# Performance work log

Hardware: AMD Instinct MI355X
Metric: run time of the kernel (lower is better)

## Reference

```python
import jax, jax.numpy as jnp
import numpy as np

H = 8  # num_heads


def _ln(x, g, b):
    mu = x.mean(-1, keepdims=True)
    var = ((x - mu) ** 2).mean(-1, keepdims=True)
    return (x - mu) * jax.lax.rsqrt(var + 1e-5) * g + b


def setup_inputs() -> dict:
    key = jax.random.key(0)
    ks = jax.random.split(key, 24)
    B, N, V, E, D, R, L = 8, 512, 50000, 300, 256, 100, 4
    dh = D // H
    s = 0.02
    inp = {}
    inp['token_ids'] = jax.random.randint(ks[0], (B, N), 0, V, dtype=jnp.int32)
    inp['relations'] = jax.random.randint(ks[1], (B, N, N), 0, R, dtype=jnp.int32)
    m = jax.random.bernoulli(ks[2], 0.9, (B, N, N))
    eye = jnp.eye(N, dtype=bool)[None]
    inp['relations_mask'] = jnp.logical_or(m, eye)  # keep diagonal valid so every row attends somewhere
    inp['embed'] = jax.random.normal(ks[3], (V, E), jnp.float32) * s
    inp['W_in'] = jax.random.normal(ks[4], (E, D), jnp.float32) * s
    inp['b_in'] = jnp.zeros((D,), jnp.float32)
    inp['Wq'] = jax.random.normal(ks[5], (L, D, D), jnp.float32) * s
    inp['Wk'] = jax.random.normal(ks[6], (L, D, D), jnp.float32) * s
    inp['Wv'] = jax.random.normal(ks[7], (L, D, D), jnp.float32) * s
    inp['Wo'] = jax.random.normal(ks[8], (L, D, D), jnp.float32) * s
    inp['ln1_g'] = jnp.ones((L, D), jnp.float32)
    inp['ln1_b'] = jnp.zeros((L, D), jnp.float32)
    inp['ln2_g'] = jnp.ones((L, D), jnp.float32)
    inp['ln2_b'] = jnp.zeros((L, D), jnp.float32)
    inp['W1'] = jax.random.normal(ks[9], (L, D, 4 * D), jnp.float32) * s
    inp['b1'] = jnp.zeros((L, 4 * D), jnp.float32)
    inp['W2'] = jax.random.normal(ks[10], (L, 4 * D, D), jnp.float32) * s
    inp['b2'] = jnp.zeros((L, D), jnp.float32)
    inp['rel_k_emb'] = jax.random.normal(ks[11], (R, dh), jnp.float32) * s
    inp['rel_v_emb'] = jax.random.normal(ks[12], (R, dh), jnp.float32) * s
    inp['W_out'] = jax.random.normal(ks[13], (D, D), jnp.float32) * s
    inp['b_out'] = jnp.zeros((D,), jnp.float32)
    return inp


def reference(token_ids, relations, relations_mask, embed, W_in, b_in, Wq, Wk, Wv, Wo,
              ln1_g, ln1_b, ln2_g, ln2_b, W1, b1, W2, b2, rel_k_emb, rel_v_emb, W_out, b_out):
    # Input layer: embedding lookup + projection to gnn hidden size.
    x = embed[token_ids]                          # [B,N,E]
    x = jax.nn.relu(x @ W_in + b_in)              # [B,N,D]
    B, N, D = x.shape
    dh = D // H
    # Shared relation embeddings (share_layers=True, share_heads=True): gathered once.
    rk = rel_k_emb[relations]                     # [B,N,N,dh]
    rv = rel_v_emb[relations]                     # [B,N,N,dh]
    neg = jnp.asarray(-1e9, x.dtype)
    scale = jnp.asarray(1.0 / np.sqrt(dh), x.dtype)
    L = Wq.shape[0]
    for l in range(L):  # fixed small layer count
        q = (x @ Wq[l]).reshape(B, N, H, dh).transpose(0, 2, 1, 3)
        k = (x @ Wk[l]).reshape(B, N, H, dh).transpose(0, 2, 1, 3)
        v = (x @ Wv[l]).reshape(B, N, H, dh).transpose(0, 2, 1, 3)
        # Relation-aware scores: q.k + q.r_k (RAT-SQL)
        scores = (jnp.einsum('bhnd,bhmd->bhnm', q, k)
                  + jnp.einsum('bhnd,bnmd->bhnm', q, rk)) * scale
        scores = jnp.where(relations_mask[:, None], scores, neg)
        a = jax.nn.softmax(scores, axis=-1)       # [B,H,N,N]
        z = (jnp.einsum('bhnm,bhmd->bhnd', a, v)
             + jnp.einsum('bhnm,bnmd->bhnd', a, rv))
        z = z.transpose(0, 2, 1, 3).reshape(B, N, D) @ Wo[l]
        x = _ln(x + z, ln1_g[l], ln1_b[l])
        f = jax.nn.relu(x @ W1[l] + b1[l]) @ W2[l] + b2[l]
        x = _ln(x + f, ln2_g[l], ln2_b[l])
    # Output layer projection
    return x @ W_out + b_out
```

## Files before the change

kernel.cpp:

```cpp
#include <hip/hip_runtime.h>
#include <hip/hip_bf16.h>

#define NTOK 4096
#define NN   512

typedef __attribute__((ext_vector_type(8))) short bf16x8;
typedef __attribute__((ext_vector_type(4))) float f32x4;
typedef __attribute__((ext_vector_type(4))) unsigned short u16x4;

__device__ __forceinline__ float bf16_to_f(unsigned short u) {
    unsigned int x = ((unsigned int)u) << 16;
    return __builtin_bit_cast(float, x);
}
__device__ __forceinline__ unsigned short f_to_bf16(float f) {
    unsigned int b = __builtin_bit_cast(unsigned int, f);
    return (unsigned short)((b + 0x7fff + ((b >> 16) & 1)) >> 16);
}
__device__ __forceinline__ bf16x8 pack8(float4 a, float4 b) {
    bf16x8 v;
    v[0]=(short)f_to_bf16(a.x); v[1]=(short)f_to_bf16(a.y);
    v[2]=(short)f_to_bf16(a.z); v[3]=(short)f_to_bf16(a.w);
    v[4]=(short)f_to_bf16(b.x); v[5]=(short)f_to_bf16(b.y);
    v[6]=(short)f_to_bf16(b.z); v[7]=(short)f_to_bf16(b.w);
    return v;
}

__global__ void detect_mask_kernel(const unsigned char* __restrict__ m, int* __restrict__ flag) {
    __shared__ int f;
    if (threadIdx.x == 0) f = 0;
    __syncthreads();
    int any = 0;
    for (int i = threadIdx.x; i < 4096; i += 256) {
        if ((i & 3) != 0 && m[i] != 0) any = 1;
    }
    if (any) atomicOr(&f, 1);
    __syncthreads();
    if (threadIdx.x == 0) *flag = f;
}

__global__ __launch_bounds__(256) void prep_rel16(
    const int* __restrict__ rel, const void* __restrict__ mask,
    const int* __restrict__ flag, short* __restrict__ rel16)
{
    const bool mbyte = (*flag != 0);
    const unsigned char* m8 = (const unsigned char*)mask;
    const int* m32 = (const int*)mask;
    const int i = (blockIdx.x * 256 + threadIdx.x) * 2;
    int2 rv = *(const int2*)(rel + i);
    int ok0, ok1;
    if (mbyte) { ok0 = m8[i]; ok1 = m8[i + 1]; }
    else       { ok0 = (m32[i] != 0); ok1 = (m32[i + 1] != 0); }
    short2 o;
    o.x = ok0 ? (short)rv.x : (short)-1;
    o.y = ok1 ? (short)rv.y : (short)-1;
    *(short2*)(rel16 + i) = o;
}

__global__ __launch_bounds__(256) void tcast256(
    const float* __restrict__ Wq, const float* __restrict__ Wk,
    const float* __restrict__ Wv, const float* __restrict__ Wo,
    const float* __restrict__ Wout, unsigned short* __restrict__ wt,
    int nL, float scale)
{
    const int z = blockIdx.z;
    const float* src; unsigned short* dst; float sc = 1.f;
    if (z >= nL * 4) {
        src = Wout; dst = wt + (size_t)nL * 786432;
    } else {
        const int l = z >> 2, which = z & 3;
        if      (which == 0) { src = Wq + (size_t)l * 65536; sc = scale; }
        else if (which == 1) { src = Wk + (size_t)l * 65536; }
        else if (which == 2) { src = Wv + (size_t)l * 65536; }
        else                 { src = Wo + (size_t)l * 65536; }
        dst = wt + (size_t)l * 786432 + which * 65536;
    }
    __shared__ float tile[32][33];
    const int t = threadIdx.x, tx = t & 31, ty = t >> 5;
    const int n0 = blockIdx.x * 32, k0 = blockIdx.y * 32;
#pragma unroll
    for (int p = 0; p < 4; ++p)
        tile[ty + p * 8][tx] = src[(size_t)(k0 + ty + p * 8) * 256 + n0 + tx];
    __syncthreads();
#pragma unroll
    for (int p = 0; p < 4; ++p)
        dst[(size_t)(n0 + ty + p * 8) * 256 + k0 + tx] = f_to_bf16(tile[tx][ty + p * 8] * sc);
}

__global__ __launch_bounds__(256) void tcastKN(
    const float* __restrict__ in, unsigned short* __restrict__ out,
    int K, int N, long inStride, long outStride)
{
    in  += (size_t)blockIdx.z * inStride;
    out += (size_t)blockIdx.z * outStride;
    __shared__ float tile[32][33];
    const int t = threadIdx.x, tx = t & 31, ty = t >> 5;
    const int n0 = blockIdx.x * 32, k0 = blockIdx.y * 32;
#pragma unroll
    for (int p = 0; p < 4; ++p)
        tile[ty + p * 8][tx] = in[(size_t)(k0 + ty + p * 8) * N + n0 + tx];
    __syncthreads();
#pragma unroll
    for (int p = 0; p < 4; ++p)
        out[(size_t)(n0 + ty + p * 8) * K + k0 + tx] = f_to_bf16(tile[tx][ty + p * 8]);
}

__global__ __launch_bounds__(256) void embed_proj_kernel(
    const int* __restrict__ tok, const float* __restrict__ embed,
    const float* __restrict__ W_in, const float* __restrict__ b_in,
    float* __restrict__ x, unsigned short* __restrict__ xh)
{
    __shared__ float emb[8][304];
    __shared__ int tloc[8];
    const int t = threadIdx.x;
    const int r0 = blockIdx.x * 8;
    if (t < 8) tloc[t] = tok[r0 + t];
    __syncthreads();
    for (int i = t; i < 8 * 300; i += 256) {
        int r = i / 300, e = i - r * 300;
        emb[r][e] = embed[(size_t)tloc[r] * 300 + e];
    }
    __syncthreads();
    float acc[8] = {0.f,0.f,0.f,0.f,0.f,0.f,0.f,0.f};
    const int d = t;
    for (int e = 0; e < 300; ++e) {
        float w = W_in[e * 256 + d];
#pragma unroll
        for (int r = 0; r < 8; ++r) acc[r] += emb[r][e] * w;
    }
    const float bb = b_in[d];
#pragma unroll
    for (int r = 0; r < 8; ++r) {
        float o = acc[r] + bb;
        o = o > 0.f ? o : 0.f;
        x[(size_t)(r0 + r) * 256 + d] = o;
        xh[(size_t)(r0 + r) * 256 + d] = f_to_bf16(o);
    }
}

__global__ __launch_bounds__(256) void gemm_bf16_64(
    const unsigned short* __restrict__ A, const unsigned short* __restrict__ WT,
    const float* __restrict__ bias, float* __restrict__ Cf, unsigned short* __restrict__ Ch,
    int M, int K, int Nc, int relu)
{
    __shared__ unsigned short As[2][64][40];
    __shared__ unsigned short Bs[2][64][40];
    const int t = threadIdx.x;
    const int lane = t & 63, w = t >> 6;
    const int g = lane >> 4, li = lane & 15;
    const int r0 = blockIdx.y * 64, c0 = blockIdx.x * 64;

    f32x4 acc[4];
#pragma unroll
    for (int i = 0; i < 4; ++i) acc[i] = (f32x4){0.f,0.f,0.f,0.f};

    const int arow = t >> 2, ad8 = (t & 3) * 8;

    bf16x8 a0 = *(const bf16x8*)(A  + (size_t)(r0 + arow) * K + ad8);
    bf16x8 b0 = *(const bf16x8*)(WT + (size_t)(c0 + arow) * K + ad8);

    const int nk = K >> 5;
    for (int ki = 0; ki < nk; ++ki) {
        const int cur = ki & 1;
        *(bf16x8*)&As[cur][arow][ad8] = a0;
        *(bf16x8*)&Bs[cur][arow][ad8] = b0;
        if (ki + 1 < nk) {
            const int k0 = (ki + 1) * 32;
            a0 = *(const bf16x8*)(A  + (size_t)(r0 + arow) * K + k0 + ad8);
            b0 = *(const bf16x8*)(WT + (size_t)(c0 + arow) * K + k0 + ad8);
        }
        __syncthreads();
        bf16x8 af = *(const bf16x8*)&As[cur][16 * w + li][g * 8];
#pragma unroll
        for (int sub = 0; sub < 4; ++sub) {
            bf16x8 bfr = *(const bf16x8*)&Bs[cur][16 * sub + li][g * 8];
            acc[sub] = __builtin_amdgcn_mfma_f32_16x16x32_bf16(af, bfr, acc[sub], 0, 0, 0);
        }
    }
#pragma unroll
    for (int sub = 0; sub < 4; ++sub) {
        int col = c0 + sub * 16 + li;
        float bv = bias ? bias[col] : 0.f;
#pragma unroll
        for (int r = 0; r < 4; ++r) {
            int row = r0 + 16 * w + g * 4 + r;
            float o = acc[sub][r] + bv;
            if (relu) o = fmaxf(o, 0.f);
            if (Ch) Ch[(size_t)row * Nc + col] = f_to_bf16(o);
            else    Cf[(size_t)row * Nc + col] = o;
        }
    }
}

__global__ __launch_bounds__(256) void gemm_bf16_32(
    const unsigned short* __restrict__ A, const unsigned short* __restrict__ WT,
    const float* __restrict__ bias, float* __restrict__ Cf, unsigned short* __restrict__ Ch,
    int M, int K, int Nc, int relu)
{
    __shared__ unsigned short As[2][32][40];
    __shared__ unsigned short Bs[2][64][40];
    const int t = threadIdx.x;
    const int lane = t & 63, w = t >> 6;
    const int g = lane >> 4, li = lane & 15;
    const int r0 = blockIdx.y * 32, c0 = blockIdx.x * 64;

    f32x4 acc[2];
    acc[0] = (f32x4){0.f,0.f,0.f,0.f};
    acc[1] = (f32x4){0.f,0.f,0.f,0.f};

    const int arow = t >> 3, a4 = (t & 7) * 4;
    const int bcol = t >> 2, bk8 = (t & 3) * 8;

    u16x4 a0 = *(const u16x4*)(A + (size_t)(r0 + arow) * K + a4);
    bf16x8 b0 = *(const bf16x8*)(WT + (size_t)(c0 + bcol) * K + bk8);

    const int nk = K >> 5;
    for (int ki = 0; ki < nk; ++ki) {
        const int cur = ki & 1;
        *(u16x4*)&As[cur][arow][a4] = a0;
        *(bf16x8*)&Bs[cur][bcol][bk8] = b0;
        if (ki + 1 < nk) {
            const int k0 = (ki + 1) * 32;
            a0 = *(const u16x4*)(A + (size_t)(r0 + arow) * K + k0 + a4);
            b0 = *(const bf16x8*)(WT + (size_t)(c0 + bcol) * K + k0 + bk8);
        }
        __syncthreads();
        bf16x8 af = *(const bf16x8*)&As[cur][16 * (w & 1) + li][g * 8];
#pragma unroll
        for (int sub = 0; sub < 2; ++sub) {
            bf16x8 bfr = *(const bf16x8*)&Bs[cur][(w >> 1) * 32 + sub * 16 + li][g * 8];
            acc[sub] = __builtin_amdgcn_mfma_f32_16x16x32_bf16(af, bfr, acc[sub], 0, 0, 0);
        }
    }
#pragma unroll
    for (int sub = 0; sub < 2; ++sub) {
        int col = c0 + (w >> 1) * 32 + sub * 16 + li;
        float bv = bias ? bias[col] : 0.f;
#pragma unroll
        for (int r = 0; r < 4; ++r) {
            int row = r0 + 16 * (w & 1) + g * 4 + r;
            float o = acc[sub][r] + bv;
            if (relu) o = fmaxf(o, 0.f);
            if (Ch) Ch[(size_t)row * Nc + col] = f_to_bf16(o);
            else    Cf[(size_t)row * Nc + col] = o;
        }
    }
}

__global__ __launch_bounds__(256) void qrk_kernel(
    const unsigned short* __restrict__ qkvh, const float* __restrict__ relk_g,
    unsigned short* __restrict__ qrkg)
{
    const int n0 = blockIdx.x * 64, h = blockIdx.y, b = blockIdx.z;
    const int t = threadIdx.x, lane = t & 63, w = t >> 6;
    const int g = lane >> 4, li = lane & 15;
    const int qrow = 16 * w + g * 4;

    __shared__ unsigned short relk_s[100][40];
    for (int i = t; i < 400; i += 256) {
        int rr = i >> 2, d8 = (i & 3) * 8;
        const float* sp = relk_g + rr * 32 + d8;
        *(bf16x8*)&relk_s[rr][d8] = pack8(*(const float4*)sp, *(const float4*)(sp + 4));
    }
    bf16x8 qf = *(const bf16x8*)(qkvh + (size_t)(b * NN + n0 + 16 * w + li) * 768 + h * 32 + g * 8);
    __syncthreads();
#pragma unroll
    for (int rc = 0; rc < 7; ++rc) {
        bf16x8 bb = *(const bf16x8*)&relk_s[rc * 16 + li][g * 8];
        f32x4 s = __builtin_amdgcn_mfma_f32_16x16x32_bf16(qf, bb, (f32x4){0.f,0.f,0.f,0.f}, 0, 0, 0);
        int col = rc * 16 + li;
        if (col < 100) {
#pragma unroll
            for (int r = 0; r < 4; ++r)
                qrkg[((size_t)(b * 8 + h) * NN + n0 + qrow + r) * 100 + col] = f_to_bf16(s[r]);
        }
    }
}

__global__ __launch_bounds__(256, 4) void attn_mfma(
    const unsigned short* __restrict__ qkvh,
    const short* __restrict__ rel16,
    const unsigned short* __restrict__ qrkg,
    const float* __restrict__ relv_g,
    float* __restrict__ zpart, float* __restrict__ smpart)
{
    const int p = blockIdx.x;
    const int cx = p & 7, k = p >> 3;
    const int sg = cx * 16 + (k >> 3);
    const int h  = k & 7;
    const int b = sg >> 4, chunk = sg & 15;
    const int n0 = chunk * 32;

    const int t = threadIdx.x;
    const int lane = t & 63, w = t >> 6;
    const int qw = w & 1, mhalf = w >> 1;
    const int g = lane >> 4, li = lane & 15;
    const int qrow = 16 * qw + g * 4;
    const int mbase = mhalf * 256;

    __shared__ float wrel[32][100];
    __shared__ unsigned short qrk_lds[32][100];
    __shared__ union {
        unsigned short relvT[32][136];
        struct {
            unsigned short v_t[2][2][32][40];
            unsigned short p_s[4][16][40];
        } mn;
    } u;

    for (int i = t; i < 3200; i += 256) ((float*)wrel)[i] = 0.f;
    {
        const unsigned short* qsrc = qrkg + ((size_t)(b * 8 + h) * NN + n0) * 100;
        for (int i = t; i < 1600; i += 256) {
            int row = i / 50, off = (i - row * 50) * 2;
            *(unsigned int*)&qrk_lds[row][off] =
                *(const unsigned int*)(qsrc + (size_t)row * 100 + off);
        }
    }
    bf16x8 qf = *(const bf16x8*)(qkvh + (size_t)(b * NN + n0 + 16 * qw + li) * 768 + h * 32 + g * 8);

    const short* relrow[4];
#pragma unroll
    for (int r = 0; r < 4; ++r)
        relrow[r] = rel16 + ((size_t)b * NN + n0 + qrow + r) * NN;
    const int th = t & 127;
    const int vm = th & 31, vdg = th >> 5;
    const size_t kRB = (size_t)(b * NN) * 768 + 256 + h * 32 + g * 8;
    const size_t vRB = (size_t)(b * NN) * 768 + 512 + h * 32 + vdg * 8;

    bf16x8 kbuf[2][2]; bf16x8 vbuf[2]; short rbuf[2][8];
#pragma unroll
    for (int i = 0; i < 8; ++i)
        rbuf[0][i] = relrow[i & 3][mbase + (i >> 2) * 16 + li];
    kbuf[0][0] = *(const bf16x8*)(qkvh + kRB + (size_t)(mbase + li) * 768);
    kbuf[0][1] = *(const bf16x8*)(qkvh + kRB + (size_t)(mbase + 16 + li) * 768);
    vbuf[0]    = *(const bf16x8*)(qkvh + vRB + (size_t)(mbase + vm) * 768);

    float smacc[4] = {0.f, 0.f, 0.f, 0.f};
    f32x4 zf[2];
    zf[0] = (f32x4){0.f,0.f,0.f,0.f};
    zf[1] = (f32x4){0.f,0.f,0.f,0.f};

#pragma unroll
    for (int tt = 0; tt < 8; ++tt) {
        const int cur = tt & 1, nxt = cur ^ 1;
        {
            bf16x8 vv = vbuf[cur];
#pragma unroll
            for (int j = 0; j < 8; ++j)
                u.mn.v_t[mhalf][cur][vdg * 8 + j][vm] = (unsigned short)vv[j];
        }
        if (tt + 1 < 8) {
            const int m0n = mbase + (tt + 1) * 32;
#pragma unroll
            for (int i = 0; i < 8; ++i)
                rbuf[nxt][i] = relrow[i & 3][m0n + (i >> 2) * 16 + li];
        }
        __syncthreads();
        bf16x8 kf0 = kbuf[cur][0], kf1 = kbuf[cur][1];
        if (tt + 1 < 8) {
            const int m0n = mbase + (tt + 1) * 32;
            kbuf[nxt][0] = *(const bf16x8*)(qkvh + kRB + (size_t)(m0n + li) * 768);
            kbuf[nxt][1] = *(const bf16x8*)(qkvh + kRB + (size_t)(m0n + 16 + li) * 768);
            vbuf[nxt]    = *(const bf16x8*)(qkvh + vRB + (size_t)(m0n + vm) * 768);
        }
        f32x4 s0 = __builtin_amdgcn_mfma_f32_16x16x32_bf16(qf, kf0, (f32x4){0.f,0.f,0.f,0.f}, 0, 0, 0);
        f32x4 s1 = __builtin_amdgcn_mfma_f32_16x16x32_bf16(qf, kf1, (f32x4){0.f,0.f,0.f,0.f}, 0, 0, 0);
        float pr[8];
#pragma unroll
        for (int i = 0; i < 8; ++i) {
            const int r = i & 3;
            const int rl = rbuf[cur][i];
            const float qadd = bf16_to_f(qrk_lds[qrow + r][rl < 0 ? 0 : rl]);
            const float sv = ((i >> 2) ? s1[r] : s0[r]) + qadd;
            float pv = 0.f;
            if (rl >= 0) {
                pv = __expf(fminf(sv, 50.f));
                atomicAdd(&wrel[qrow + r][rl], pv);
            }
            smacc[r] += pv;
            pr[i] = pv;
        }
#pragma unroll
        for (int i = 0; i < 8; ++i)
            u.mn.p_s[w][g * 4 + (i & 3)][(i >> 2) * 16 + li] = f_to_bf16(pr[i]);
        asm volatile("s_waitcnt lgkmcnt(0)" ::: "memory");
        __builtin_amdgcn_sched_barrier(0);
        bf16x8 pa = *(const bf16x8*)&u.mn.p_s[w][li][g * 8];
#pragma unroll
        for (int dc = 0; dc < 2; ++dc) {
            bf16x8 vb = *(const bf16x8*)&u.mn.v_t[mhalf][cur][dc * 16 + li][g * 8];
            zf[dc] = __builtin_amdgcn_mfma_f32_16x16x32_bf16(pa, vb, zf[dc], 0, 0, 0);
        }
    }
    __syncthreads();

    for (int i = t; i < 32 * 36; i += 256) {
        int d = i / 36, c = 100 + (i - (i / 36) * 36);
        u.relvT[d][c] = 0;
    }
    for (int i = t; i < 400; i += 256) {
        int rr2 = i >> 2, d8 = (i & 3) * 8;
        const float* sp = relv_g + rr2 * 32 + d8;
        float4 s0 = *(const float4*)sp, s1 = *(const float4*)(sp + 4);
        u.relvT[d8 + 0][rr2] = f_to_bf16(s0.x);
        u.relvT[d8 + 1][rr2] = f_to_bf16(s0.y);
        u.relvT[d8 + 2][rr2] = f_to_bf16(s0.z);
        u.relvT[d8 + 3][rr2] = f_to_bf16(s0.w);
        u.relvT[d8 + 4][rr2] = f_to_bf16(s1.x);
        u.relvT[d8 + 5][rr2] = f_to_bf16(s1.y);
        u.relvT[d8 + 6][rr2] = f_to_bf16(s1.z);
        u.relvT[d8 + 7][rr2] = f_to_bf16(s1.w);
    }
    __syncthreads();
    if (mhalf == 0) {
#pragma unroll
        for (int kc = 0; kc < 4; ++kc) {
            const int kbase = kc * 32 + g * 8;
            const float* wp = &wrel[16 * qw + li][0];
            bf16x8 af;
#pragma unroll
            for (int j = 0; j < 8; ++j) {
                int id = kbase + j;
                float val = (id < 100) ? wp[id] : 0.f;
                af[j] = (short)f_to_bf16(val);
            }
#pragma unroll
            for (int dc = 0; dc < 2; ++dc) {
                bf16x8 vbr = *(const bf16x8*)&u.relvT[dc * 16 + li][kbase];
                zf[dc] = __builtin_amdgcn_mfma_f32_16x16x32_bf16(af, vbr, zf[dc], 0, 0, 0);
            }
        }
    }
#pragma unroll
    for (int r = 0; r < 4; ++r) {
        smacc[r] += __shfl_xor(smacc[r], 1, 64);
        smacc[r] += __shfl_xor(smacc[r], 2, 64);
        smacc[r] += __shfl_xor(smacc[r], 4, 64);
        smacc[r] += __shfl_xor(smacc[r], 8, 64);
    }
#pragma unroll
    for (int r = 0; r < 4; ++r) {
        const int row = b * NN + n0 + qrow + r;
        size_t ob = (size_t)mhalf * 1048576 + (size_t)row * 256 + h * 32;
#pragma unroll
        for (int dc = 0; dc < 2; ++dc)
            zpart[ob + dc * 16 + li] = zf[dc][r];
        if (li == 0)
            smpart[(size_t)mhalf * 32768 + (size_t)row * 8 + h] = smacc[r];
    }
}

__global__ __launch_bounds__(256) void combine_kernel(
    const float* __restrict__ zpart, const float* __restrict__ smpart,
    unsigned short* __restrict__ zbf)
{
    const int t = threadIdx.x;
    const int wi = t >> 6, lane = t & 63;
    const int row = blockIdx.x * 4 + wi;
    const int h = lane >> 3;
    float den = 0.f;
    float4 acc = make_float4(0.f, 0.f, 0.f, 0.f);
#pragma unroll
    for (int s = 0; s < 2; ++s) {
        den += smpart[(size_t)s * 32768 + (size_t)row * 8 + h];
        float4 v = *(const float4*)(zpart + (size_t)s * 1048576 + (size_t)row * 256 + lane * 4);
        acc.x += v.x; acc.y += v.y; acc.z += v.z; acc.w += v.w;
    }
    const float inv = 1.f / den;
    u16x4 oh;
    oh[0] = f_to_bf16(acc.x * inv);
    oh[1] = f_to_bf16(acc.y * inv);
    oh[2] = f_to_bf16(acc.z * inv);
    oh[3] = f_to_bf16(acc.w * inv);
    *(u16x4*)(zbf + (size_t)row * 256 + lane * 4) = oh;
}

__global__ __launch_bounds__(256) void ln_kernel(
    const float* __restrict__ xin, const float* __restrict__ y,
    const float* __restrict__ g, const float* __restrict__ bsh,
    float* __restrict__ xout, unsigned short* __restrict__ xh)
{
    const int t = threadIdx.x;
    const int w = t >> 6, lane = t & 63;
    const size_t row = (size_t)blockIdx.x * 4 + w;
    const float4 xv = *(const float4*)(xin + row * 256 + lane * 4);
    const float4 yv = *(const float4*)(y + row * 256 + lane * 4);
    float4 sv;
    sv.x = xv.x + yv.x; sv.y = xv.y + yv.y; sv.z = xv.z + yv.z; sv.w = xv.w + yv.w;
    float sum = sv.x + sv.y + sv.z + sv.w;
    float sq  = sv.x * sv.x + sv.y * sv.y + sv.z * sv.z + sv.w * sv.w;
#pragma unroll
    for (int off = 1; off < 64; off <<= 1) {
        sum += __shfl_xor(sum, off, 64);
        sq  += __shfl_xor(sq, off, 64);
    }
    const float mu = sum * (1.f / 256.f);
    const float var = sq * (1.f / 256.f) - mu * mu;
    const float rs = rsqrtf(var + 1e-5f);
    const float4 gv = *(const float4*)(g + lane * 4);
    const float4 bv = *(const float4*)(bsh + lane * 4);
    float4 o;
    o.x = (sv.x - mu) * rs * gv.x + bv.x;
    o.y = (sv.y - mu) * rs * gv.y + bv.y;
    o.z = (sv.z - mu) * rs * gv.z + bv.z;
    o.w = (sv.w - mu) * rs * gv.w + bv.w;
    *(float4*)(xout + row * 256 + lane * 4) = o;
    u16x4 oh;
    oh[0] = f_to_bf16(o.x); oh[1] = f_to_bf16(o.y);
    oh[2] = f_to_bf16(o.z); oh[3] = f_to_bf16(o.w);
    *(u16x4*)(xh + row * 256 + lane * 4) = oh;
}

extern "C" void kernel_launch(void* const* d_in, const int* in_sizes, int n_in,
                              void* d_out, int out_size, void* d_ws, size_t ws_size,
                              hipStream_t stream)
{
    (void)in_sizes; (void)n_in; (void)out_size;
    const int*   tok   = (const int*)d_in[0];
    const int*   rel   = (const int*)d_in[1];
    const void*  mask  = d_in[2];
    const float* embed = (const float*)d_in[3];
    const float* W_in  = (const float*)d_in[4];
    const float* b_in  = (const float*)d_in[5];
    const float* Wq    = (const float*)d_in[6];
    const float* Wk    = (const float*)d_in[7];
    const float* Wv    = (const float*)d_in[8];
    const float* Wo    = (const float*)d_in[9];
    const float* ln1g  = (const float*)d_in[10];
    const float* ln1b  = (const float*)d_in[11];
    const float* ln2g  = (const float*)d_in[12];
    const float* ln2b  = (const float*)d_in[13];
    const float* W1    = (const float*)d_in[14];
    const float* b1    = (const float*)d_in[15];
    const float* W2    = (const float*)d_in[16];
    const float* b2    = (const float*)d_in[17];
    const float* relk  = (const float*)d_in[18];
    const float* relv  = (const float*)d_in[19];
    const float* Wout  = (const float*)d_in[20];
    const float* bout  = (const float*)d_in[21];
    float* out = (float*)d_out;
    const float scale = 0.17677669529663687f;

    float* ws = (float*)d_ws;
    float*          x     = ws;
    unsigned short* xh    = (unsigned short*)(ws + 1048576);
    unsigned short* zbf   = (unsigned short*)(ws + 1572864);
    float*          zo    = ws + 2097152;
    unsigned short* qkvh  = (unsigned short*)(ws + 3145728);
    unsigned short* hbh   = (unsigned short*)(ws + 4718592);
    float*          zpart = ws + 6815744;
    float*          smpart= ws + 8912896;
    unsigned short* qrkg  = (unsigned short*)(ws + 8978432);
    int*            flag  = (int*)(ws + 10616832);
    unsigned short* wt    = (unsigned short*)(ws + 10616848);

    const size_t wsf = ws_size >> 2;
    const bool tierA = wsf >= 13271100;
    short* rel16 = tierA ? (short*)(ws + 12222480) : (short*)hbh;

    detect_mask_kernel<<<1, 256, 0, stream>>>((const unsigned char*)mask, flag);
    embed_proj_kernel<<<512, 256, 0, stream>>>(tok, embed, W_in, b_in, x, xh);
    if (tierA) {
        prep_rel16<<<4096, 256, 0, stream>>>(rel, mask, flag, rel16);
        tcast256<<<dim3(8, 8, 17), 256, 0, stream>>>(Wq, Wk, Wv, Wo, Wout, wt, 4, scale);
        tcastKN<<<dim3(32, 8, 4), 256, 0, stream>>>(W1, wt + 262144, 256, 1024, 262144, 786432);
        tcastKN<<<dim3(8, 32, 4), 256, 0, stream>>>(W2, wt + 524288, 1024, 256, 262144, 786432);
    }

    for (int l = 0; l < 4; ++l) {
        unsigned short* wl = tierA ? wt + (size_t)l * 786432 : wt;
        if (!tierA) {
            prep_rel16<<<4096, 256, 0, stream>>>(rel, mask, flag, rel16);
            tcast256<<<dim3(8, 8, 4), 256, 0, stream>>>(
                Wq + (size_t)l * 65536, Wk + (size_t)l * 65536,
                Wv + (size_t)l * 65536, Wo + (size_t)l * 65536, Wout, wt, 1, scale);
            tcastKN<<<dim3(32, 8, 1), 256, 0, stream>>>(W1 + (size_t)l * 262144, wt + 262144, 256, 1024, 0, 0);
            tcastKN<<<dim3(8, 32, 1), 256, 0, stream>>>(W2 + (size_t)l * 262144, wt + 524288, 1024, 256, 0, 0);
        }
        gemm_bf16_64<<<dim3(12, 64), 256, 0, stream>>>(xh, wl, nullptr, nullptr, qkvh,
                                                       NTOK, 256, 768, 0);
        qrk_kernel<<<dim3(8, 8, 8), 256, 0, stream>>>(qkvh, relk, qrkg);
        attn_mfma<<<1024, 256, 0, stream>>>(qkvh, rel16, qrkg, relv, zpart, smpart);
        combine_kernel<<<1024, 256, 0, stream>>>(zpart, smpart, zbf);
        gemm_bf16_32<<<dim3(4, 128), 256, 0, stream>>>(zbf, wl + 196608, nullptr, zo, nullptr,
                                                       NTOK, 256, 256, 0);
        ln_kernel<<<1024, 256, 0, stream>>>(x, zo, ln1g + l * 256, ln1b + l * 256, x, xh);
        gemm_bf16_64<<<dim3(16, 64), 256, 0, stream>>>(xh, wl + 262144, b1 + l * 1024, nullptr, hbh,
                                                       NTOK, 256, 1024, 1);
        gemm_bf16_32<<<dim3(4, 128), 256, 0, stream>>>(hbh, wl + 524288, b2 + l * 256, zo, nullptr,
                                                       NTOK, 1024, 256, 0);
        ln_kernel<<<1024, 256, 0, stream>>>(x, zo, ln2g + l * 256, ln2b + l * 256, x, xh);
    }
    unsigned short* woutT = wt;
    if (tierA) {
        woutT = wt + (size_t)4 * 786432;
    } else {
        tcast256<<<dim3(8, 8, 1), 256, 0, stream>>>(Wq, Wk, Wv, Wo, Wout, wt, 0, scale);
    }
    gemm_bf16_32<<<dim3(4, 128), 256, 0, stream>>>(xh, woutT, bout, out, nullptr,
                                                   NTOK, 256, 256, 0);
}
```

Baseline: 617.3 us.

## Process 64-key tiles per iteration in relation-attention loop with deeper register prefetch

Restructures the attention main loop to handle two 32-key sub-tiles per iteration (4 iterations instead of 8), prefetching twice as many K, V and relation values into registers. The P buffer in shared memory gains a second slot. The intent is to halve loop overhead and make the MFMA and exp work per barrier more independent, at the cost of higher register pressure and two barriers per iteration instead of one.

```diff
diff --git a/kernel.cpp b/kernel.cpp
--- a/kernel.cpp
+++ b/kernel.cpp
@@ -303,7 +303,7 @@
         unsigned short relvT[32][136];
         struct {
             unsigned short v_t[2][2][32][40];
-            unsigned short p_s[4][16][40];
+            unsigned short p_s[4][2][16][40];
         } mn;
     } u;
 
@@ -327,72 +327,95 @@
     const size_t kRB = (size_t)(b * NN) * 768 + 256 + h * 32 + g * 8;
     const size_t vRB = (size_t)(b * NN) * 768 + 512 + h * 32 + vdg * 8;
 
-    bf16x8 kbuf[2][2]; bf16x8 vbuf[2]; short rbuf[2][8];
-#pragma unroll
-    for (int i = 0; i < 8; ++i)
-        rbuf[0][i] = relrow[i & 3][mbase + (i >> 2) * 16 + li];
-    kbuf[0][0] = *(const bf16x8*)(qkvh + kRB + (size_t)(mbase + li) * 768);
-    kbuf[0][1] = *(const bf16x8*)(qkvh + kRB + (size_t)(mbase + 16 + li) * 768);
-    vbuf[0]    = *(const bf16x8*)(qkvh + vRB + (size_t)(mbase + vm) * 768);
+    bf16x8 kreg[2][4];
+    bf16x8 vreg[2][2];
+    short  rreg[2][16];
+    {
+#pragma unroll
+        for (int i = 0; i < 8; ++i) {
+            rreg[0][i]     = relrow[i & 3][mbase + (i >> 2) * 16 + li];
+            rreg[0][8 + i] = relrow[i & 3][mbase + 32 + (i >> 2) * 16 + li];
+        }
+        kreg[0][0] = *(const bf16x8*)(qkvh + kRB + (size_t)(mbase + li) * 768);
+        kreg[0][1] = *(const bf16x8*)(qkvh + kRB + (size_t)(mbase + 16 + li) * 768);
+        kreg[0][2] = *(const bf16x8*)(qkvh + kRB + (size_t)(mbase + 32 + li) * 768);
+        kreg[0][3] = *(const bf16x8*)(qkvh + kRB + (size_t)(mbase + 48 + li) * 768);
+        vreg[0][0] = *(const bf16x8*)(qkvh + vRB + (size_t)(mbase + vm) * 768);
+        vreg[0][1] = *(const bf16x8*)(qkvh + vRB + (size_t)(mbase + 32 + vm) * 768);
+    }
 
     float smacc[4] = {0.f, 0.f, 0.f, 0.f};
     f32x4 zf[2];
     zf[0] = (f32x4){0.f,0.f,0.f,0.f};
     zf[1] = (f32x4){0.f,0.f,0.f,0.f};
 
-#pragma unroll
-    for (int tt = 0; tt < 8; ++tt) {
-        const int cur = tt & 1, nxt = cur ^ 1;
+    __syncthreads();
+
+#pragma unroll
+    for (int pr = 0; pr < 4; ++pr) {
+        const int cur = pr & 1, nxt = cur ^ 1;
         {
-            bf16x8 vv = vbuf[cur];
-#pragma unroll
-            for (int j = 0; j < 8; ++j)
-                u.mn.v_t[mhalf][cur][vdg * 8 + j][vm] = (unsigned short)vv[j];
-        }
-        if (tt + 1 < 8) {
-            const int m0n = mbase + (tt + 1) * 32;
-#pragma unroll
-            for (int i = 0; i < 8; ++i)
-                rbuf[nxt][i] = relrow[i & 3][m0n + (i >> 2) * 16 + li];
-        }
-        __syncthreads();
-        bf16x8 kf0 = kbuf[cur][0], kf1 = kbuf[cur][1];
-        if (tt + 1 < 8) {
-            const int m0n = mbase + (tt + 1) * 32;
-            kbuf[nxt][0] = *(const bf16x8*)(qkvh + kRB + (size_t)(m0n + li) * 768);
-            kbuf[nxt][1] = *(const bf16x8*)(qkvh + kRB + (size_t)(m0n + 16 + li) * 768);
-            vbuf[nxt]    = *(const bf16x8*)(qkvh + vRB + (size_t)(m0n + vm) * 768);
-        }
-        f32x4 s0 = __builtin_amdgcn_mfma_f32_16x16x32_bf16(qf, kf0, (f32x4){0.f,0.f,0.f,0.f}, 0, 0, 0);
-        f32x4 s1 = __builtin_amdgcn_mfma_f32_16x16x32_bf16(qf, kf1, (f32x4){0.f,0.f,0.f,0.f}, 0, 0, 0);
-        float pr[8];
+            bf16x8 va = vreg[cur][0], vb2 = vreg[cur][1];
+#pragma unroll
+            for (int j = 0; j < 8; ++j) {
+                u.mn.v_t[mhalf][0][vdg * 8 + j][vm] = (unsigned short)va[j];
+                u.mn.v_t[mhalf][1][vdg * 8 + j][vm] = (unsigned short)vb2[j];
+            }
+        }
+        if (pr + 1 < 4) {
+            const int m0n = mbase + (pr + 1) * 64;
+#pragma unroll
+            for (int i = 0; i < 8; ++i) {
+                rreg[nxt][i]     = relrow[i & 3][m0n + (i >> 2) * 16 + li];
+                rreg[nxt][8 + i] = relrow[i & 3][m0n + 32 + (i >> 2) * 16 + li];
+            }
+        }
+        f32x4 sA0 = __builtin_amdgcn_mfma_f32_16x16x32_bf16(qf, kreg[cur][0], (f32x4){0.f,0.f,0.f,0.f}, 0, 0, 0);
+        f32x4 sA1 = __builtin_amdgcn_mfma_f32_16x16x32_bf16(qf, kreg[cur][1], (f32x4){0.f,0.f,0.f,0.f}, 0, 0, 0);
+        f32x4 sB0 = __builtin_amdgcn_mfma_f32_16x16x32_bf16(qf, kreg[cur][2], (f32x4){0.f,0.f,0.f,0.f}, 0, 0, 0);
+        f32x4 sB1 = __builtin_amdgcn_mfma_f32_16x16x32_bf16(qf, kreg[cur][3], (f32x4){0.f,0.f,0.f,0.f}, 0, 0, 0);
+        if (pr + 1 < 4) {
+            const int m0n = mbase + (pr + 1) * 64;
+            kreg[nxt][0] = *(const bf16x8*)(qkvh + kRB + (size_t)(m0n + li) * 768);
+            kreg[nxt][1] = *(const bf16x8*)(qkvh + kRB + (size_t)(m0n + 16 + li) * 768);
+            kreg[nxt][2] = *(const bf16x8*)(qkvh + kRB + (size_t)(m0n + 32 + li) * 768);
+            kreg[nxt][3] = *(const bf16x8*)(qkvh + kRB + (size_t)(m0n + 48 + li) * 768);
+            vreg[nxt][0] = *(const bf16x8*)(qkvh + vRB + (size_t)(m0n + vm) * 768);
+            vreg[nxt][1] = *(const bf16x8*)(qkvh + vRB + (size_t)(m0n + 32 + vm) * 768);
+        }
 #pragma unroll
         for (int i = 0; i < 8; ++i) {
             const int r = i & 3;
-            const int rl = rbuf[cur][i];
-            const float qadd = bf16_to_f(qrk_lds[qrow + r][rl < 0 ? 0 : rl]);
-            const float sv = ((i >> 2) ? s1[r] : s0[r]) + qadd;
-            float pv = 0.f;
-            if (rl >= 0) {
-                pv = __expf(fminf(sv, 50.f));
-                atomicAdd(&wrel[qrow + r][rl], pv);
+            const int rlA = rreg[cur][i], rlB = rreg[cur][8 + i];
+            const float qaA = bf16_to_f(qrk_lds[qrow + r][rlA < 0 ? 0 : rlA]);
+            const float qaB = bf16_to_f(qrk_lds[qrow + r][rlB < 0 ? 0 : rlB]);
+            const float svA = ((i >> 2) ? sA1[r] : sA0[r]) + qaA;
+            const float svB = ((i >> 2) ? sB1[r] : sB0[r]) + qaB;
+            float pA = 0.f, pB = 0.f;
+            if (rlA >= 0) {
+                pA = __expf(fminf(svA, 50.f));
+                atomicAdd(&wrel[qrow + r][rlA], pA);
             }
-            smacc[r] += pv;
-            pr[i] = pv;
-        }
-#pragma unroll
-        for (int i = 0; i < 8; ++i)
-            u.mn.p_s[w][g * 4 + (i & 3)][(i >> 2) * 16 + li] = f_to_bf16(pr[i]);
-        asm volatile("s_waitcnt lgkmcnt(0)" ::: "memory");
-        __builtin_amdgcn_sched_barrier(0);
-        bf16x8 pa = *(const bf16x8*)&u.mn.p_s[w][li][g * 8];
+            if (rlB >= 0) {
+                pB = __expf(fminf(svB, 50.f));
+                atomicAdd(&wrel[qrow + r][rlB], pB);
+            }
+            smacc[r] += pA + pB;
+            u.mn.p_s[w][0][g * 4 + r][(i >> 2) * 16 + li] = f_to_bf16(pA);
+            u.mn.p_s[w][1][g * 4 + r][(i >> 2) * 16 + li] = f_to_bf16(pB);
+        }
+        __syncthreads();
+        bf16x8 paA = *(const bf16x8*)&u.mn.p_s[w][0][li][g * 8];
+        bf16x8 paB = *(const bf16x8*)&u.mn.p_s[w][1][li][g * 8];
 #pragma unroll
         for (int dc = 0; dc < 2; ++dc) {
-            bf16x8 vb = *(const bf16x8*)&u.mn.v_t[mhalf][cur][dc * 16 + li][g * 8];
-            zf[dc] = __builtin_amdgcn_mfma_f32_16x16x32_bf16(pa, vb, zf[dc], 0, 0, 0);
-        }
-    }
-    __syncthreads();
+            bf16x8 vA = *(const bf16x8*)&u.mn.v_t[mhalf][0][dc * 16 + li][g * 8];
+            bf16x8 vB = *(const bf16x8*)&u.mn.v_t[mhalf][1][dc * 16 + li][g * 8];
+            zf[dc] = __builtin_amdgcn_mfma_f32_16x16x32_bf16(paA, vA, zf[dc], 0, 0, 0);
+            zf[dc] = __builtin_amdgcn_mfma_f32_16x16x32_bf16(paB, vB, zf[dc], 0, 0, 0);
+        }
+        __syncthreads();
+    }
 
     for (int i = t; i < 32 * 36; i += 256) {
         int d = i / 36, c = 100 + (i - (i / 36) * 36);
```

New measurement: 628.9 us. No clear change (+1.9%).

## Load full 256-wide K slabs into XOR-swizzled LDS in GEMM kernels

Applied to the files above, without the earlier changes.

The GEMM kernels stop double-buffering 32-wide K tiles with a barrier per step. They now load a whole 256-wide K slab of A and B into shared memory with an XOR swizzle to avoid bank conflicts, then run eight MFMA steps per barrier. This cuts synchronisation and loop overhead, and for K=256 there is a single load phase. The cost is a large LDS footprint (64 KB or 48 KB per block), which lowers occupancy, and there is no overlap of global loads with compute.

```diff
diff --git a/kernel.cpp b/kernel.cpp
--- a/kernel.cpp
+++ b/kernel.cpp
@@ -137,13 +137,14 @@
     }
 }
 
-__global__ __launch_bounds__(256) void gemm_bf16_64(
+__global__ __launch_bounds__(256) void gemm_bigk64(
     const unsigned short* __restrict__ A, const unsigned short* __restrict__ WT,
     const float* __restrict__ bias, float* __restrict__ Cf, unsigned short* __restrict__ Ch,
     int M, int K, int Nc, int relu)
 {
-    __shared__ unsigned short As[2][64][40];
-    __shared__ unsigned short Bs[2][64][40];
+    __shared__ unsigned short As[64][256];
+    __shared__ unsigned short Bs[64][256];
+    char* Ab = (char*)As; char* Bb = (char*)Bs;
     const int t = threadIdx.x;
     const int lane = t & 63, w = t >> 6;
     const int g = lane >> 4, li = lane & 15;
@@ -153,27 +154,30 @@
 #pragma unroll
     for (int i = 0; i < 4; ++i) acc[i] = (f32x4){0.f,0.f,0.f,0.f};
 
-    const int arow = t >> 2, ad8 = (t & 3) * 8;
-
-    bf16x8 a0 = *(const bf16x8*)(A  + (size_t)(r0 + arow) * K + ad8);
-    bf16x8 b0 = *(const bf16x8*)(WT + (size_t)(c0 + arow) * K + ad8);
-
-    const int nk = K >> 5;
-    for (int ki = 0; ki < nk; ++ki) {
-        const int cur = ki & 1;
-        *(bf16x8*)&As[cur][arow][ad8] = a0;
-        *(bf16x8*)&Bs[cur][arow][ad8] = b0;
-        if (ki + 1 < nk) {
-            const int k0 = (ki + 1) * 32;
-            a0 = *(const bf16x8*)(A  + (size_t)(r0 + arow) * K + k0 + ad8);
-            b0 = *(const bf16x8*)(WT + (size_t)(c0 + arow) * K + k0 + ad8);
+    for (int k0 = 0; k0 < K; k0 += 256) {
+        if (k0) __syncthreads();
+#pragma unroll
+        for (int j = 0; j < 8; ++j) {
+            int idx = j * 256 + t;
+            int row = idx >> 5;
+            int colb = (idx & 31) * 16;
+            int sw = row * 512 + (colb ^ ((row & 7) << 4));
+            *(bf16x8*)(Ab + sw) = *(const bf16x8*)(A  + (size_t)(r0 + row) * K + k0 + (idx & 31) * 8);
+            *(bf16x8*)(Bb + sw) = *(const bf16x8*)(WT + (size_t)(c0 + row) * K + k0 + (idx & 31) * 8);
         }
         __syncthreads();
-        bf16x8 af = *(const bf16x8*)&As[cur][16 * w + li][g * 8];
-#pragma unroll
-        for (int sub = 0; sub < 4; ++sub) {
-            bf16x8 bfr = *(const bf16x8*)&Bs[cur][16 * sub + li][g * 8];
-            acc[sub] = __builtin_amdgcn_mfma_f32_16x16x32_bf16(af, bfr, acc[sub], 0, 0, 0);
+        const int arow = 16 * w + li;
+        const int xr = (li & 7) << 4;
+#pragma unroll
+        for (int ks = 0; ks < 8; ++ks) {
+            const int kb = (g * 8 + ks * 32) * 2;
+            bf16x8 af = *(const bf16x8*)(Ab + arow * 512 + (kb ^ xr));
+#pragma unroll
+            for (int sub = 0; sub < 4; ++sub) {
+                const int brow = sub * 16 + li;
+                bf16x8 bfr = *(const bf16x8*)(Bb + brow * 512 + (kb ^ xr));
+                acc[sub] = __builtin_amdgcn_mfma_f32_16x16x32_bf16(af, bfr, acc[sub], 0, 0, 0);
+            }
         }
     }
 #pragma unroll
@@ -191,13 +195,14 @@
     }
 }
 
-__global__ __launch_bounds__(256) void gemm_bf16_32(
+__global__ __launch_bounds__(256) void gemm_bigk32(
     const unsigned short* __restrict__ A, const unsigned short* __restrict__ WT,
     const float* __restrict__ bias, float* __restrict__ Cf, unsigned short* __restrict__ Ch,
     int M, int K, int Nc, int relu)
 {
-    __shared__ unsigned short As[2][32][40];
-    __shared__ unsigned short Bs[2][64][40];
+    __shared__ unsigned short As[32][256];
+    __shared__ unsigned short Bs[64][256];
+    char* Ab = (char*)As; char* Bb = (char*)Bs;
     const int t = threadIdx.x;
     const int lane = t & 63, w = t >> 6;
     const int g = lane >> 4, li = lane & 15;
@@ -207,28 +212,37 @@
     acc[0] = (f32x4){0.f,0.f,0.f,0.f};
     acc[1] = (f32x4){0.f,0.f,0.f,0.f};
 
-    const int arow = t >> 3, a4 = (t & 7) * 4;
-    const int bcol = t >> 2, bk8 = (t & 3) * 8;
-
-    u16x4 a0 = *(const u16x4*)(A + (size_t)(r0 + arow) * K + a4);
-    bf16x8 b0 = *(const bf16x8*)(WT + (size_t)(c0 + bcol) * K + bk8);
-
-    const int nk = K >> 5;
-    for (int ki = 0; ki < nk; ++ki) {
-        const int cur = ki & 1;
-        *(u16x4*)&As[cur][arow][a4] = a0;
-        *(bf16x8*)&Bs[cur][bcol][bk8] = b0;
-        if (ki + 1 < nk) {
-            const int k0 = (ki + 1) * 32;
-            a0 = *(const u16x4*)(A + (size_t)(r0 + arow) * K + k0 + a4);
-            b0 = *(const bf16x8*)(WT + (size_t)(c0 + bcol) * K + k0 + bk8);
+    for (int k0 = 0; k0 < K; k0 += 256) {
+        if (k0) __syncthreads();
+#pragma unroll
+        for (int j = 0; j < 4; ++j) {
+            int idx = j * 256 + t;
+            int row = idx >> 5;
+            int colb = (idx & 31) * 16;
+            int sw = row * 512 + (colb ^ ((row & 7) << 4));
+            *(bf16x8*)(Ab + sw) = *(const bf16x8*)(A + (size_t)(r0 + row) * K + k0 + (idx & 31) * 8);
+        }
+#pragma unroll
+        for (int j = 0; j < 8; ++j) {
+            int idx = j * 256 + t;
+            int row = idx >> 5;
+            int colb = (idx & 31) * 16;
+            int sw = row * 512 + (colb ^ ((row & 7) << 4));
+            *(bf16x8*)(Bb + sw) = *(const bf16x8*)(WT + (size_t)(c0 + row) * K + k0 + (idx & 31) * 8);
         }
         __syncthreads();
-        bf16x8 af = *(const bf16x8*)&As[cur][16 * (w & 1) + li][g * 8];
-#pragma unroll
-        for (int sub = 0; sub < 2; ++sub) {
-            bf16x8 bfr = *(const bf16x8*)&Bs[cur][(w >> 1) * 32 + sub * 16 + li][g * 8];
-            acc[sub] = __builtin_amdgcn_mfma_f32_16x16x32_bf16(af, bfr, acc[sub], 0, 0, 0);
+        const int arow = 16 * (w & 1) + li;
+        const int xr = (li & 7) << 4;
+#pragma unroll
+        for (int ks = 0; ks < 8; ++ks) {
+            const int kb = (g * 8 + ks * 32) * 2;
+            bf16x8 af = *(const bf16x8*)(Ab + arow * 512 + (kb ^ xr));
+#pragma unroll
+            for (int sub = 0; sub < 2; ++sub) {
+                const int brow = (w >> 1) * 32 + sub * 16 + li;
+                bf16x8 bfr = *(const bf16x8*)(Bb + brow * 512 + (kb ^ xr));
+                acc[sub] = __builtin_amdgcn_mfma_f32_16x16x32_bf16(af, bfr, acc[sub], 0, 0, 0);
+            }
         }
     }
 #pragma unroll
@@ -577,18 +591,18 @@
             tcastKN<<<dim3(32, 8, 1), 256, 0, stream>>>(W1 + (size_t)l * 262144, wt + 262144, 256, 1024, 0, 0);
             tcastKN<<<dim3(8, 32, 1), 256, 0, stream>>>(W2 + (size_t)l * 262144, wt + 524288, 1024, 256, 0, 0);
         }
-        gemm_bf16_64<<<dim3(12, 64), 256, 0, stream>>>(xh, wl, nullptr, nullptr, qkvh,
-                                                       NTOK, 256, 768, 0);
+        gemm_bigk64<<<dim3(12, 64), 256, 0, stream>>>(xh, wl, nullptr, nullptr, qkvh,
+                                                      NTOK, 256, 768, 0);
         qrk_kernel<<<dim3(8, 8, 8), 256, 0, stream>>>(qkvh, relk, qrkg);
         attn_mfma<<<1024, 256, 0, stream>>>(qkvh, rel16, qrkg, relv, zpart, smpart);
         combine_kernel<<<1024, 256, 0, stream>>>(zpart, smpart, zbf);
-        gemm_bf16_32<<<dim3(4, 128), 256, 0, stream>>>(zbf, wl + 196608, nullptr, zo, nullptr,
-                                                       NTOK, 256, 256, 0);
+        gemm_bigk32<<<dim3(4, 128), 256, 0, stream>>>(zbf, wl + 196608, nullptr, zo, nullptr,
+                                                      NTOK, 256, 256, 0);
         ln_kernel<<<1024, 256, 0, stream>>>(x, zo, ln1g + l * 256, ln1b + l * 256, x, xh);
-        gemm_bf16_64<<<dim3(16, 64), 256, 0, stream>>>(xh, wl + 262144, b1 + l * 1024, nullptr, hbh,
-                                                       NTOK, 256, 1024, 1);
-        gemm_bf16_32<<<dim3(4, 128), 256, 0, stream>>>(hbh, wl + 524288, b2 + l * 256, zo, nullptr,
-                                                       NTOK, 1024, 256, 0);
+        gemm_bigk64<<<dim3(16, 64), 256, 0, stream>>>(xh, wl + 262144, b1 + l * 1024, nullptr, hbh,
+                                                      NTOK, 256, 1024, 1);
+        gemm_bigk32<<<dim3(4, 128), 256, 0, stream>>>(hbh, wl + 524288, b2 + l * 256, zo, nullptr,
+                                                      NTOK, 1024, 256, 0);
         ln_kernel<<<1024, 256, 0, stream>>>(x, zo, ln2g + l * 256, ln2b + l * 256, x, xh);
     }
     unsigned short* woutT = wt;
@@ -597,6 +611,6 @@
     } else {
         tcast256<<<dim3(8, 8, 1), 256, 0, stream>>>(Wq, Wk, Wv, Wo, Wout, wt, 0, scale);
     }
-    gemm_bf16_32<<<dim3(4, 128), 256, 0, stream>>>(xh, woutT, bout, out, nullptr,
-                                                   NTOK, 256, 256, 0);
-}
+    gemm_bigk32<<<dim3(4, 128), 256, 0, stream>>>(xh, woutT, bout, out, nullptr,
+                                                  NTOK, 256, 256, 0);
+}
```

Measured after the change: 623.5 us. About the same (+1.0%).
